# Kernel optimization log

Hardware: AMD Instinct MI355X
Metric: run time of the kernel (lower is better)

The kernel has to match this reference:

```python
import jax, jax.numpy as jnp
import numpy as np

B, S, H, NH = 2, 2048, 1024, 16
HD = H // NH  # head_dim = 64
ROPE_BASE = 10000.0


def _rope(x):
    # x: [B, NH, S, HD]; LLaMA-style half-split rotary embedding
    s, d = x.shape[2], x.shape[3]
    inv_freq = 1.0 / (ROPE_BASE ** (jnp.arange(0, d, 2, dtype=jnp.float32) / d))  # [d/2]
    ang = jnp.arange(s, dtype=jnp.float32)[:, None] * inv_freq[None, :]            # [S, d/2]
    cos, sin = jnp.cos(ang), jnp.sin(ang)
    x1, x2 = x[..., : d // 2], x[..., d // 2:]
    return jnp.concatenate([x1 * cos - x2 * sin, x1 * sin + x2 * cos], axis=-1)


def setup_inputs() -> dict:
    key = jax.random.key(0)
    ks = jax.random.split(key, 9)
    hidden_states = jax.random.normal(ks[0], (B, S, H), dtype=jnp.float32)
    # causal mask: True = attend
    causal = jnp.tril(jnp.ones((S, S), dtype=bool))
    attention_mask = jnp.broadcast_to(causal[None, None, :, :], (B, 1, S, S))
    std = 0.02
    wq = jax.random.normal(ks[1], (H, NH * HD), dtype=jnp.float32) * std
    wk = jax.random.normal(ks[2], (H, NH * HD), dtype=jnp.float32) * std
    wv = jax.random.normal(ks[3], (H, NH * HD), dtype=jnp.float32) * std
    wo = jax.random.normal(ks[4], (NH * HD, H), dtype=jnp.float32) * std
    bq = jnp.zeros((NH * HD,), dtype=jnp.float32)
    bk = jnp.zeros((NH * HD,), dtype=jnp.float32)
    bv = jnp.zeros((NH * HD,), dtype=jnp.float32)
    bo = jnp.zeros((H,), dtype=jnp.float32)
    return {"hidden_states": hidden_states, "attention_mask": attention_mask,
            "wq": wq, "bq": bq, "wk": wk, "bk": bk, "wv": wv, "bv": bv,
            "wo": wo, "bo": bo}


def _split_heads(x):
    b, s, _ = x.shape
    return jnp.transpose(x.reshape(b, s, NH, HD), (0, 2, 1, 3))


def reference(hidden_states, attention_mask, wq, bq, wk, bk, wv, bv, wo, bo):
    q = _split_heads(hidden_states @ wq + bq)  # [B,NH,S,HD]
    k = _split_heads(hidden_states @ wk + bk)
    v = _split_heads(hidden_states @ wv + bv)
    q = _rope(q)
    k = _rope(k)
    scores = jnp.einsum('bhqd,bhkd->bhqk', q, k) / jnp.sqrt(jnp.float32(HD))
    scores = jnp.where(attention_mask, scores, jnp.float32(-1e9))
    weights = jax.nn.softmax(scores, axis=-1)
    attn = jnp.einsum('bhqk,bhkv->bhqv', weights, v)  # [B,NH,S,HD]
    attn = jnp.transpose(attn, (0, 2, 1, 3)).reshape(hidden_states.shape[0], attn.shape[2], H)
    return attn @ wo + bo
```

## Files before the change

### kernel.cpp

```cpp
#include <hip/hip_runtime.h>
#include <math.h>

typedef short bf16x8 __attribute__((ext_vector_type(8)));
typedef short bf16x4 __attribute__((ext_vector_type(4)));
typedef float f32x4  __attribute__((ext_vector_type(4)));

__device__ __forceinline__ unsigned short f2bf(float f) {
    union { float f; unsigned u; } v; v.f = f;
    unsigned r = v.u + 0x7FFFu + ((v.u >> 16) & 1u);
    return (unsigned short)(r >> 16);
}

__device__ __forceinline__ unsigned cvt_pk_bf16(float a, float b) {
    unsigned r;
    asm("v_cvt_pk_bf16_f32 %0, %1, %2" : "=v"(r) : "v"(a), "v"(b));
    return r;
}

#define GLDS16(gp, lp) __builtin_amdgcn_global_load_lds( \
    (const __attribute__((address_space(1))) void*)(gp), \
    (__attribute__((address_space(3))) void*)(lp), 16, 0, 0)


__global__ __launch_bounds__(256)
void prep(const float* __restrict__ X, unsigned short* __restrict__ Xb,
          const float* __restrict__ w0, const float* __restrict__ w1,
          const float* __restrict__ w2, const float* __restrict__ w3,
          unsigned short* o0, unsigned short* o1,
          unsigned short* o2, unsigned short* o3)
{
    const int z = blockIdx.z;
    if (z >= 4) {
        const int lb = (z - 4) * 256 + blockIdx.y * 16 + blockIdx.x;
        const size_t t = (size_t)lb * 256 + threadIdx.x;
        const float4 a = *(const float4*)(X + t * 8);
        const float4 b = *(const float4*)(X + t * 8 + 4);
        unsigned short u[8] = { f2bf(a.x), f2bf(a.y), f2bf(a.z), f2bf(a.w),
                                f2bf(b.x), f2bf(b.y), f2bf(b.z), f2bf(b.w) };
        *(int4*)(Xb + t * 8) = *(int4*)u;
        return;
    }
    const float* W; unsigned short* O;
    switch (z) {
        case 0: W = w0; O = o0; break;
        case 1: W = w1; O = o1; break;
        case 2: W = w2; O = o2; break;
        default: W = w3; O = o3; break;
    }
    __shared__ float T[64][65];
    const int tid = threadIdx.x;
    const int n0 = blockIdx.x * 64, k0 = blockIdx.y * 64;
    #pragma unroll
    for (int i = 0; i < 4; i++) {
        const int k = (tid >> 4) + i * 16, n4 = (tid & 15) * 4;
        const float4 v = *(const float4*)(W + (size_t)(k0 + k) * 1024 + n0 + n4);
        T[k][n4] = v.x; T[k][n4+1] = v.y; T[k][n4+2] = v.z; T[k][n4+3] = v.w;
    }
    __syncthreads();
    if (z == 3) {
        #pragma unroll
        for (int i = 0; i < 4; i++) {
            const int n = (tid >> 4) + i * 16, k4 = (tid & 15) * 4;
            unsigned short u[4];
            #pragma unroll
            for (int j = 0; j < 4; j++) {
                const int q = k4 + j;
                const int p = (q & 3) * 16 + (q >> 2);
                const int d = (p & 3) * 16 + (p >> 2);
                u[j] = f2bf(T[d][n]);
            }
            *(int2*)(O + (size_t)(n0 + n) * 1024 + k0 + k4) = *(int2*)u;
        }
    } else {
        #pragma unroll
        for (int i = 0; i < 4; i++) {
            const int n = (tid >> 4) + i * 16, k4 = (tid & 15) * 4;
            unsigned short u[4] = { f2bf(T[k4][n]), f2bf(T[k4+1][n]),
                                    f2bf(T[k4+2][n]), f2bf(T[k4+3][n]) };
            *(int2*)(O + (size_t)(n0 + n) * 1024 + k0 + k4) = *(int2*)u;
        }
    }
}

__global__ __launch_bounds__(256)
void qkv_gemm(const unsigned short* __restrict__ Xb,
              const unsigned short* __restrict__ Wtq, const unsigned short* __restrict__ Wtk,
              const unsigned short* __restrict__ Wtv,
              const float* __restrict__ bq, const float* __restrict__ bk,
              const float* __restrict__ bv,
              unsigned short* __restrict__ Qb, unsigned short* __restrict__ Kb,
              unsigned short* __restrict__ Vtb)
{
    const unsigned short* Wt; const float* bias; unsigned short* Out;
    const int z = blockIdx.z;
    if (z == 0)      { Wt = Wtq; bias = bq; Out = Qb; }
    else if (z == 1) { Wt = Wtk; bias = bk; Out = Kb; }
    else             { Wt = Wtv; bias = bv; Out = Vtb; }

    __shared__ unsigned short Sh[128 * 72];
    unsigned short* As = Sh;
    unsigned short* Bs = Sh + 128 * 32;
    unsigned short* T  = Sh;

    const int tid = threadIdx.x, lane = tid & 63, w = tid >> 6;
    const int quad = lane >> 4, c = lane & 15;
    const int wr = w >> 1, wc = w & 1;
    const int m0 = blockIdx.x * 128, n0 = blockIdx.y * 128;
    const int srow = lane >> 2, scol = (lane & 3) * 8;

    f32x4 acc[4][4];
    #pragma unroll
    for (int i = 0; i < 4; i++)
        #pragma unroll
        for (int j = 0; j < 4; j++) acc[i][j] = (f32x4){0.f, 0.f, 0.f, 0.f};

    for (int k0 = 0; k0 < 1024; k0 += 32) {
        #pragma unroll
        for (int j = 0; j < 2; j++) {
            const int r = w * 32 + j * 16;
            GLDS16(Xb + (size_t)(m0 + r + srow) * 1024 + k0 + scol, &As[r * 32]);
            GLDS16(Wt + (size_t)(n0 + r + srow) * 1024 + k0 + scol, &Bs[r * 32]);
        }
        __syncthreads();
        bf16x8 af[4], bf[4];
        #pragma unroll
        for (int rt = 0; rt < 4; rt++)
            af[rt] = *(const bf16x8*)&As[(wr * 64 + rt * 16 + c) * 32 + quad * 8];
        #pragma unroll
        for (int nt = 0; nt < 4; nt++)
            bf[nt] = *(const bf16x8*)&Bs[(wc * 64 + nt * 16 + c) * 32 + quad * 8];
        #pragma unroll
        for (int rt = 0; rt < 4; rt++)
            #pragma unroll
            for (int nt = 0; nt < 4; nt++)
                acc[rt][nt] = __builtin_amdgcn_mfma_f32_16x16x32_bf16(af[rt], bf[nt], acc[rt][nt], 0, 0, 0);
        __syncthreads();
    }

    float bv4[4];
    #pragma unroll
    for (int nt = 0; nt < 4; nt++) bv4[nt] = bias[n0 + wc * 64 + nt * 16 + c];

    if (z == 2) {
        const int b = m0 >> 11, sb = m0 & 2047;
        const int hgbase = n0 >> 6;
        #pragma unroll
        for (int h = 0; h < 2; h++) {
            if (wc == h) {
                #pragma unroll
                for (int rt = 0; rt < 4; rt++)
                    #pragma unroll
                    for (int reg = 0; reg < 4; reg++) {
                        const int s = wr * 64 + rt * 16 + quad * 4 + reg;
                        unsigned short u[4];
                        #pragma unroll
                        for (int nt = 0; nt < 4; nt++)
                            u[nt] = f2bf(acc[rt][nt][reg] + bv4[nt]);
                        *(int2*)&T[s * 72 + c * 4] = *(int2*)u;
                    }
            }
            __syncthreads();
            const int p = tid >> 2, s8 = (tid & 3) * 32;
            unsigned short* dstb = Vtb + ((size_t)(b * 16 + hgbase + h) * 64 + p) * 2048 + sb;
            #pragma unroll
            for (int jj = 0; jj < 32; jj += 8) {
                unsigned short u[8];
                #pragma unroll
                for (int j = 0; j < 8; j++) u[j] = T[(s8 + jj + j) * 72 + p];
                *(int4*)(dstb + s8 + jj) = *(int4*)u;
            }
            __syncthreads();
        }
        return;
    }

    const float kLn = 9.210340371976184f / 32.0f;
    const float TWO_PI_INV = 0.15915494309189535f;
    const float rv0 = expf(-(float)c * kLn) * TWO_PI_INV;
    const float rv1 = expf(-(float)(c + 16) * kLn) * TWO_PI_INV;
    const float qscale = (z == 0) ? 0.125f : 1.0f;

    #pragma unroll
    for (int rt = 0; rt < 4; rt++) {
        #pragma unroll
        for (int reg = 0; reg < 4; reg++) {
            const int m = m0 + wr * 64 + rt * 16 + quad * 4 + reg;
            const int b = m >> 11, s = m & 2047;
            float x0 = acc[rt][0][reg] + bv4[0];
            float x1 = acc[rt][1][reg] + bv4[1];
            float x2 = acc[rt][2][reg] + bv4[2];
            float x3 = acc[rt][3][reg] + bv4[3];
            float r0 = (float)s * rv0;  r0 -= floorf(r0);
            float r1 = (float)s * rv1;  r1 -= floorf(r1);
            const float sn0 = __builtin_amdgcn_sinf(r0);
            const float cs0 = __builtin_amdgcn_cosf(r0);
            const float sn1 = __builtin_amdgcn_sinf(r1);
            const float cs1 = __builtin_amdgcn_cosf(r1);
            const float y0 = (x0 * cs0 - x2 * sn0) * qscale;
            const float y2 = (x0 * sn0 + x2 * cs0) * qscale;
            const float y1 = (x1 * cs1 - x3 * sn1) * qscale;
            const float y3 = (x1 * sn1 + x3 * cs1) * qscale;
            const int h = (n0 + wc * 64) >> 6;
            unsigned short u[4] = { f2bf(y0), f2bf(y1), f2bf(y2), f2bf(y3) };
            unsigned short* dst = Out + ((size_t)(b * 16 + h) * 2048 + s) * 64;
            *(int2*)(dst + c * 4) = *(int2*)u;
        }
    }
}

__global__ __launch_bounds__(256)
void out_gemm(const unsigned short* __restrict__ Ab, const unsigned short* __restrict__ Wto,
              const float* __restrict__ bo, float* __restrict__ Out)
{
    __shared__ unsigned short As[64 * 32];
    __shared__ unsigned short Bs[128 * 32];
    const int tid = threadIdx.x, lane = tid & 63, w = tid >> 6;
    const int quad = lane >> 4, c = lane & 15;
    const int wr = w >> 1, wc = w & 1;
    const int m0 = blockIdx.x * 64, n0 = blockIdx.y * 128;
    const int srow = lane >> 2, scol = (lane & 3) * 8;

    f32x4 acc[2][4];
    #pragma unroll
    for (int i = 0; i < 2; i++)
        #pragma unroll
        for (int j = 0; j < 4; j++) acc[i][j] = (f32x4){0.f, 0.f, 0.f, 0.f};

    for (int k0 = 0; k0 < 1024; k0 += 32) {
        {
            const int r = w * 16;
            GLDS16(Ab + (size_t)(m0 + r + srow) * 1024 + k0 + scol, &As[r * 32]);
        }
        #pragma unroll
        for (int j = 0; j < 2; j++) {
            const int r = w * 32 + j * 16;
            GLDS16(Wto + (size_t)(n0 + r + srow) * 1024 + k0 + scol, &Bs[r * 32]);
        }
        __syncthreads();
        bf16x8 af[2], bf[4];
        #pragma unroll
        for (int rt = 0; rt < 2; rt++)
            af[rt] = *(const bf16x8*)&As[(wr * 32 + rt * 16 + c) * 32 + quad * 8];
        #pragma unroll
        for (int nt = 0; nt < 4; nt++)
            bf[nt] = *(const bf16x8*)&Bs[(wc * 64 + nt * 16 + c) * 32 + quad * 8];
        #pragma unroll
        for (int rt = 0; rt < 2; rt++)
            #pragma unroll
            for (int nt = 0; nt < 4; nt++)
                acc[rt][nt] = __builtin_amdgcn_mfma_f32_16x16x32_bf16(af[rt], bf[nt], acc[rt][nt], 0, 0, 0);
        __syncthreads();
    }
    #pragma unroll
    for (int rt = 0; rt < 2; rt++) {
        #pragma unroll
        for (int reg = 0; reg < 4; reg++) {
            const int m = m0 + wr * 32 + rt * 16 + quad * 4 + reg;
            #pragma unroll
            for (int nt = 0; nt < 4; nt++) {
                const int n = n0 + wc * 64 + nt * 16 + c;
                Out[(size_t)m * 1024 + n] = acc[rt][nt][reg] + bo[n];
            }
        }
    }
}

__global__ __launch_bounds__(512)
void attn_part(const unsigned short* __restrict__ Qb, const unsigned short* __restrict__ Kb,
               const unsigned short* __restrict__ Vtb, unsigned short* __restrict__ Ab,
               float* __restrict__ Opart, float* __restrict__ Lpart)
{
    __shared__ unsigned short Ks[64 * 72];
    __shared__ unsigned short Vs[64 * 72];

    const int tid = threadIdx.x, w = tid >> 6, lane = tid & 63;
    const int quad = lane >> 4, c = lane & 15;
    const int bh = blockIdx.y;
    const int x = blockIdx.x;
    int ip, start, len;
    if (x < 8)       { ip = 9 + x;  start = 0;  len = 16; }
    else if (x < 16) { ip = 24 - x; start = 16; len = 2 * ip - 16; }
    else             { ip = 24 - x; start = 0;  len = 2 * ip; }
    const int q0 = (ip - 1) * 128;
    const bool complete = (x >= 16);
    const size_t base = (size_t)bh * 2048 * 64;

    bf16x8 on;
    #pragma unroll
    for (int i = 0; i < 8; i++) on[i] = (short)0x3F80;

    const int qbase = q0 + w * 16;
    const int qrow  = qbase + c;
    const size_t qoff = base + (size_t)qrow * 64;
    const bf16x8 qf0 = *(const bf16x8*)(Qb + qoff + quad * 8);
    const bf16x8 qf1 = *(const bf16x8*)(Qb + qoff + 32 + quad * 8);

    f32x4 O[4], Osum;
    Osum = (f32x4){0.f, 0.f, 0.f, 0.f};
    #pragma unroll
    for (int nt = 0; nt < 4; nt++) O[nt] = (f32x4){0.f, 0.f, 0.f, 0.f};

    const int rs = tid >> 3, c8 = (tid & 7) * 8;

    int k0 = start * 64;
    int4 kreg = *(const int4*)(Kb  + base + (size_t)(k0 + rs) * 64 + c8);
    int4 vreg = *(const int4*)(Vtb + base + (size_t)rs * 2048 + k0 + c8);

    union P8 { bf16x8 v8; unsigned wd[4]; };
    union V8 { bf16x8 v8; bf16x4 v4[2]; };

    for (int t = 0; t < len; t++, k0 += 64) {
        *(int4*)&Ks[(size_t)rs * 72 + c8] = kreg;
        *(int4*)&Vs[(size_t)rs * 72 + c8] = vreg;
        __syncthreads();

        if (t + 1 < len) {
            const int kn = k0 + 64;
            kreg = *(const int4*)(Kb  + base + (size_t)(kn + rs) * 64 + c8);
            vreg = *(const int4*)(Vtb + base + (size_t)rs * 2048 + kn + c8);
        }

        if (k0 <= qbase + 15) {
            const bool need_mask = (k0 + 63) > qbase;
            P8 pa0, pa1;
            __builtin_amdgcn_s_setprio(1);
            #pragma unroll
            for (int nt = 0; nt < 4; nt++) {
                const bf16x8 kf0 = *(const bf16x8*)&Ks[(nt * 16 + c) * 72 + quad * 8];
                const bf16x8 kf1 = *(const bf16x8*)&Ks[(nt * 16 + c) * 72 + 32 + quad * 8];
                f32x4 s4 = (f32x4){0.f, 0.f, 0.f, 0.f};
                s4 = __builtin_amdgcn_mfma_f32_16x16x32_bf16(kf0, qf0, s4, 0, 0, 0);
                s4 = __builtin_amdgcn_mfma_f32_16x16x32_bf16(kf1, qf1, s4, 0, 0, 0);
                const int keyb = k0 + nt * 16 + quad * 4;
                float p[4];
                #pragma unroll
                for (int reg = 0; reg < 4; reg++) {
                    float pv = __expf(s4[reg]);
                    if (need_mask && (keyb + reg > qrow)) pv = 0.f;
                    p[reg] = pv;
                }
                const unsigned wa = cvt_pk_bf16(p[0], p[1]);
                const unsigned wb = cvt_pk_bf16(p[2], p[3]);
                if (nt < 2) { pa0.wd[2 * nt]     = wa; pa0.wd[2 * nt + 1]     = wb; }
                else        { pa1.wd[2 * (nt-2)] = wa; pa1.wd[2 * (nt-2) + 1] = wb; }
            }

            #pragma unroll
            for (int nt = 0; nt < 4; nt++) {
                const int pr = (nt * 16 + c) * 72 + 4 * quad;
                V8 vb0, vb1;
                vb0.v4[0] = *(const bf16x4*)&Vs[pr];
                vb0.v4[1] = *(const bf16x4*)&Vs[pr + 16];
                vb1.v4[0] = *(const bf16x4*)&Vs[pr + 32];
                vb1.v4[1] = *(const bf16x4*)&Vs[pr + 48];
                O[nt] = __builtin_amdgcn_mfma_f32_16x16x32_bf16(pa0.v8, vb0.v8, O[nt], 0, 0, 0);
                O[nt] = __builtin_amdgcn_mfma_f32_16x16x32_bf16(pa1.v8, vb1.v8, O[nt], 0, 0, 0);
            }
            Osum = __builtin_amdgcn_mfma_f32_16x16x32_bf16(pa0.v8, on, Osum, 0, 0, 0);
            Osum = __builtin_amdgcn_mfma_f32_16x16x32_bf16(pa1.v8, on, Osum, 0, 0, 0);
            __builtin_amdgcn_s_setprio(0);
        }
        __syncthreads();
    }

    if (complete) {
        const int b = bh >> 4, h = bh & 15;
        #pragma unroll
        for (int reg = 0; reg < 4; reg++) {
            const float inv = 1.0f / Osum[reg];
            const int q = qbase + quad * 4 + reg;
            unsigned short u[4];
            #pragma unroll
            for (int nt = 0; nt < 4; nt++) u[nt] = f2bf(O[nt][reg] * inv);
            unsigned short* dst = Ab + ((size_t)(b * 2048 + q)) * 1024 + h * 64;
            *(int2*)(dst + c * 4) = *(int2*)u;
        }
    } else {
        const int pslot = (ip - 9) * 2 + (start ? 1 : 0);
        float* Op = Opart + ((size_t)bh * 16 + pslot) * 8192;
        float* Lp = Lpart + (size_t)bh * 2048 + (size_t)pslot * 128;
        #pragma unroll
        for (int reg = 0; reg < 4; reg++) {
            const int row = w * 16 + quad * 4 + reg;
            float4 o4 = make_float4(O[0][reg], O[1][reg], O[2][reg], O[3][reg]);
            *(float4*)(Op + (size_t)row * 64 + c * 4) = o4;
            if (c == 0) Lp[row] = Osum[reg];
        }
    }
}

__global__ __launch_bounds__(256)
void attn_combine(const float* __restrict__ Opart, const float* __restrict__ Lpart,
                  unsigned short* __restrict__ Ab)
{
    const int tid = threadIdx.x;
    const int j = blockIdx.x, bh = blockIdx.y;
    const int q0 = (8 + j) * 128;
    const size_t s0 = ((size_t)bh * 16 + j * 2) * 8192;
    const size_t l0 = (size_t)bh * 2048 + (size_t)j * 2 * 128;

    __shared__ float linv[128];
    if (tid < 128) linv[tid] = 1.0f / (Lpart[l0 + tid] + Lpart[l0 + 128 + tid]);
    __syncthreads();

    const int row = tid >> 1, col0 = (tid & 1) * 32;
    const float inv = linv[row];
    const int b = bh >> 4, h = bh & 15;
    const int q = q0 + row;
    unsigned short* dst = Ab + ((size_t)(b * 2048 + q)) * 1024 + h * 64 + col0;
    #pragma unroll
    for (int c4 = 0; c4 < 32; c4 += 4) {
        const float4 a  = *(const float4*)(Opart + s0 + (size_t)row * 64 + col0 + c4);
        const float4 bb = *(const float4*)(Opart + s0 + 8192 + (size_t)row * 64 + col0 + c4);
        dst[c4 + 0] = f2bf((a.x + bb.x) * inv);
        dst[c4 + 1] = f2bf((a.y + bb.y) * inv);
        dst[c4 + 2] = f2bf((a.z + bb.z) * inv);
        dst[c4 + 3] = f2bf((a.w + bb.w) * inv);
    }
}

extern "C" void kernel_launch(void* const* d_in, const int* in_sizes, int n_in,
                              void* d_out, int out_size, void* d_ws, size_t ws_size,
                              hipStream_t stream)
{
    const float* X  = (const float*)d_in[0];
    const float* wq = (const float*)d_in[2];
    const float* bq = (const float*)d_in[3];
    const float* wk = (const float*)d_in[4];
    const float* bk = (const float*)d_in[5];
    const float* wv = (const float*)d_in[6];
    const float* bv = (const float*)d_in[7];
    const float* wo = (const float*)d_in[8];
    const float* bo = (const float*)d_in[9];

    unsigned short* ws = (unsigned short*)d_ws;
    const size_t M1 = 1024 * 1024;
    unsigned short* Xb  = ws;
    unsigned short* Wtq = Xb  + 4 * M1;
    unsigned short* Wtk = Wtq + M1;
    unsigned short* Wtv = Wtk + M1;
    unsigned short* Wto = Wtv + M1;
    unsigned short* Qb  = Wto + M1;
    unsigned short* Kb  = Qb  + 4 * M1;
    unsigned short* Vtb = Kb  + 4 * M1;
    unsigned short* Ab  = Vtb + 4 * M1;
    float* Opart = (float*)(Ab + 4 * M1);
    float* Lpart = Opart + (size_t)32 * 16 * 8192;

    prep        <<<dim3(16, 16, 12), 256, 0, stream>>>(X, Xb, wq, wk, wv, wo,
                                                       Wtq, Wtk, Wtv, Wto);
    qkv_gemm    <<<dim3(32, 8, 3), 256, 0, stream>>>(Xb, Wtq, Wtk, Wtv, bq, bk, bv,
                                                     Qb, Kb, Vtb);
    attn_part   <<<dim3(24, 32), 512, 0, stream>>>(Qb, Kb, Vtb, Ab, Opart, Lpart);
    attn_combine<<<dim3(8, 32), 256, 0, stream>>>(Opart, Lpart, Ab);
    out_gemm    <<<dim3(64, 8), 256, 0, stream>>>(Ab, Wto, bo, (float*)d_out);
}
```

Measured before the change: 211.4 us.

## Double attention query tile per warp to reuse K/V tiles across 256 rows

Each warp now processes two 16-row query sub-tiles (32 rows), so each block covers 256 query rows instead of 128. Every K/V tile loaded into LDS feeds twice as many MFMAs, and the grid shrinks from 24 to 12 blocks per head, with the causal work split remapped through a packed lookup constant. The cost is more registers per thread, fewer blocks (384 total) to fill the GPU, and coarser causal load balancing. The partial-result layout and the combine kernel are adjusted to match.

```diff
diff --git a/kernel.cpp b/kernel.cpp
--- a/kernel.cpp
+++ b/kernel.cpp
@@ -277,28 +277,31 @@
     const int quad = lane >> 4, c = lane & 15;
     const int bh = blockIdx.y;
     const int x = blockIdx.x;
-    int ip, start, len;
-    if (x < 8)       { ip = 9 + x;  start = 0;  len = 16; }
-    else if (x < 16) { ip = 24 - x; start = 16; len = 2 * ip - 16; }
-    else             { ip = 24 - x; start = 0;  len = 2 * ip; }
-    const int q0 = (ip - 1) * 128;
-    const bool complete = (x >= 16);
+    const int i = (int)((0x014425566377ULL >> (4 * x)) & 15);
+    const int chunk = (594 >> x) & 1;
+    const int len = ((i >= 4) ? 2 : 4) * (i + 1);
+    const int start = chunk ? len : 0;
+    const int q0 = i * 256;
+    const bool complete = (i <= 3);
     const size_t base = (size_t)bh * 2048 * 64;
 
     bf16x8 on;
     #pragma unroll
-    for (int i = 0; i < 8; i++) on[i] = (short)0x3F80;
-
-    const int qbase = q0 + w * 16;
-    const int qrow  = qbase + c;
-    const size_t qoff = base + (size_t)qrow * 64;
-    const bf16x8 qf0 = *(const bf16x8*)(Qb + qoff + quad * 8);
-    const bf16x8 qf1 = *(const bf16x8*)(Qb + qoff + 32 + quad * 8);
-
-    f32x4 O[4], Osum;
-    Osum = (f32x4){0.f, 0.f, 0.f, 0.f};
-    #pragma unroll
-    for (int nt = 0; nt < 4; nt++) O[nt] = (f32x4){0.f, 0.f, 0.f, 0.f};
+    for (int ii = 0; ii < 8; ii++) on[ii] = (short)0x3F80;
+
+    const int qbase = q0 + w * 32;
+    const size_t qoffA = base + (size_t)(qbase + c) * 64;
+    const size_t qoffB = base + (size_t)(qbase + 16 + c) * 64;
+    const bf16x8 qfA0 = *(const bf16x8*)(Qb + qoffA + quad * 8);
+    const bf16x8 qfA1 = *(const bf16x8*)(Qb + qoffA + 32 + quad * 8);
+    const bf16x8 qfB0 = *(const bf16x8*)(Qb + qoffB + quad * 8);
+    const bf16x8 qfB1 = *(const bf16x8*)(Qb + qoffB + 32 + quad * 8);
+
+    f32x4 OA[4], OB[4], OsA, OsB;
+    OsA = (f32x4){0.f, 0.f, 0.f, 0.f};
+    OsB = (f32x4){0.f, 0.f, 0.f, 0.f};
+    #pragma unroll
+    for (int nt = 0; nt < 4; nt++) { OA[nt] = OsA; OB[nt] = OsA; }
 
     const int rs = tid >> 3, c8 = (tid & 7) * 8;
 
@@ -320,29 +323,45 @@
             vreg = *(const int4*)(Vtb + base + (size_t)rs * 2048 + kn + c8);
         }
 
-        if (k0 <= qbase + 15) {
-            const bool need_mask = (k0 + 63) > qbase;
-            P8 pa0, pa1;
+        if (k0 <= qbase + 31) {
+            const int qrowA = qbase + c;
+            const int qrowB = qbase + 16 + c;
+            const bool nmA = (k0 + 63) > qbase;
+            const bool nmB = (k0 + 63) > (qbase + 16);
+            P8 paA0, paA1, paB0, paB1;
             __builtin_amdgcn_s_setprio(1);
             #pragma unroll
             for (int nt = 0; nt < 4; nt++) {
                 const bf16x8 kf0 = *(const bf16x8*)&Ks[(nt * 16 + c) * 72 + quad * 8];
                 const bf16x8 kf1 = *(const bf16x8*)&Ks[(nt * 16 + c) * 72 + 32 + quad * 8];
-                f32x4 s4 = (f32x4){0.f, 0.f, 0.f, 0.f};
-                s4 = __builtin_amdgcn_mfma_f32_16x16x32_bf16(kf0, qf0, s4, 0, 0, 0);
-                s4 = __builtin_amdgcn_mfma_f32_16x16x32_bf16(kf1, qf1, s4, 0, 0, 0);
+                f32x4 sA = (f32x4){0.f, 0.f, 0.f, 0.f};
+                f32x4 sB = sA;
+                sA = __builtin_amdgcn_mfma_f32_16x16x32_bf16(kf0, qfA0, sA, 0, 0, 0);
+                sA = __builtin_amdgcn_mfma_f32_16x16x32_bf16(kf1, qfA1, sA, 0, 0, 0);
+                sB = __builtin_amdgcn_mfma_f32_16x16x32_bf16(kf0, qfB0, sB, 0, 0, 0);
+                sB = __builtin_amdgcn_mfma_f32_16x16x32_bf16(kf1, qfB1, sB, 0, 0, 0);
                 const int keyb = k0 + nt * 16 + quad * 4;
-                float p[4];
+                float pA[4], pB[4];
                 #pragma unroll
                 for (int reg = 0; reg < 4; reg++) {
-                    float pv = __expf(s4[reg]);
-                    if (need_mask && (keyb + reg > qrow)) pv = 0.f;
-                    p[reg] = pv;
+                    float va = __expf(sA[reg]);
+                    if (nmA && (keyb + reg > qrowA)) va = 0.f;
+                    pA[reg] = va;
+                    float vb = __expf(sB[reg]);
+                    if (nmB && (keyb + reg > qrowB)) vb = 0.f;
+                    pB[reg] = vb;
                 }
-                const unsigned wa = cvt_pk_bf16(p[0], p[1]);
-                const unsigned wb = cvt_pk_bf16(p[2], p[3]);
-                if (nt < 2) { pa0.wd[2 * nt]     = wa; pa0.wd[2 * nt + 1]     = wb; }
-                else        { pa1.wd[2 * (nt-2)] = wa; pa1.wd[2 * (nt-2) + 1] = wb; }
+                const unsigned waA = cvt_pk_bf16(pA[0], pA[1]);
+                const unsigned wbA = cvt_pk_bf16(pA[2], pA[3]);
+                const unsigned waB = cvt_pk_bf16(pB[0], pB[1]);
+                const unsigned wbB = cvt_pk_bf16(pB[2], pB[3]);
+                if (nt < 2) {
+                    paA0.wd[2 * nt] = waA;     paA0.wd[2 * nt + 1] = wbA;
+                    paB0.wd[2 * nt] = waB;     paB0.wd[2 * nt + 1] = wbB;
+                } else {
+                    paA1.wd[2 * (nt-2)] = waA; paA1.wd[2 * (nt-2) + 1] = wbA;
+                    paB1.wd[2 * (nt-2)] = waB; paB1.wd[2 * (nt-2) + 1] = wbB;
+                }
             }
 
             #pragma unroll
@@ -353,11 +372,15 @@
                 vb0.v4[1] = *(const bf16x4*)&Vs[pr + 16];
                 vb1.v4[0] = *(const bf16x4*)&Vs[pr + 32];
                 vb1.v4[1] = *(const bf16x4*)&Vs[pr + 48];
-                O[nt] = __builtin_amdgcn_mfma_f32_16x16x32_bf16(pa0.v8, vb0.v8, O[nt], 0, 0, 0);
-                O[nt] = __builtin_amdgcn_mfma_f32_16x16x32_bf16(pa1.v8, vb1.v8, O[nt], 0, 0, 0);
-            }
-            Osum = __builtin_amdgcn_mfma_f32_16x16x32_bf16(pa0.v8, on, Osum, 0, 0, 0);
-            Osum = __builtin_amdgcn_mfma_f32_16x16x32_bf16(pa1.v8, on, Osum, 0, 0, 0);
+                OA[nt] = __builtin_amdgcn_mfma_f32_16x16x32_bf16(paA0.v8, vb0.v8, OA[nt], 0, 0, 0);
+                OA[nt] = __builtin_amdgcn_mfma_f32_16x16x32_bf16(paA1.v8, vb1.v8, OA[nt], 0, 0, 0);
+                OB[nt] = __builtin_amdgcn_mfma_f32_16x16x32_bf16(paB0.v8, vb0.v8, OB[nt], 0, 0, 0);
+                OB[nt] = __builtin_amdgcn_mfma_f32_16x16x32_bf16(paB1.v8, vb1.v8, OB[nt], 0, 0, 0);
+            }
+            OsA = __builtin_amdgcn_mfma_f32_16x16x32_bf16(paA0.v8, on, OsA, 0, 0, 0);
+            OsA = __builtin_amdgcn_mfma_f32_16x16x32_bf16(paA1.v8, on, OsA, 0, 0, 0);
+            OsB = __builtin_amdgcn_mfma_f32_16x16x32_bf16(paB0.v8, on, OsB, 0, 0, 0);
+            OsB = __builtin_amdgcn_mfma_f32_16x16x32_bf16(paB1.v8, on, OsB, 0, 0, 0);
             __builtin_amdgcn_s_setprio(0);
         }
         __syncthreads();
@@ -367,24 +390,37 @@
         const int b = bh >> 4, h = bh & 15;
         #pragma unroll
         for (int reg = 0; reg < 4; reg++) {
-            const float inv = 1.0f / Osum[reg];
-            const int q = qbase + quad * 4 + reg;
-            unsigned short u[4];
-            #pragma unroll
-            for (int nt = 0; nt < 4; nt++) u[nt] = f2bf(O[nt][reg] * inv);
-            unsigned short* dst = Ab + ((size_t)(b * 2048 + q)) * 1024 + h * 64;
-            *(int2*)(dst + c * 4) = *(int2*)u;
+            const float invA = 1.0f / OsA[reg];
+            const int qA = qbase + quad * 4 + reg;
+            unsigned short uA[4];
+            #pragma unroll
+            for (int nt = 0; nt < 4; nt++) uA[nt] = f2bf(OA[nt][reg] * invA);
+            unsigned short* dA = Ab + ((size_t)(b * 2048 + qA)) * 1024 + h * 64;
+            *(int2*)(dA + c * 4) = *(int2*)uA;
+
+            const float invB = 1.0f / OsB[reg];
+            const int qB = qbase + 16 + quad * 4 + reg;
+            unsigned short uB[4];
+            #pragma unroll
+            for (int nt = 0; nt < 4; nt++) uB[nt] = f2bf(OB[nt][reg] * invB);
+            unsigned short* dB = Ab + ((size_t)(b * 2048 + qB)) * 1024 + h * 64;
+            *(int2*)(dB + c * 4) = *(int2*)uB;
         }
     } else {
-        const int pslot = (ip - 9) * 2 + (start ? 1 : 0);
-        float* Op = Opart + ((size_t)bh * 16 + pslot) * 8192;
-        float* Lp = Lpart + (size_t)bh * 2048 + (size_t)pslot * 128;
+        const int slot = (i - 4) * 2 + chunk;
+        float* Op = Opart + ((size_t)bh * 8 + slot) * 16384;
+        float* Lp = Lpart + (size_t)bh * 2048 + (size_t)slot * 256;
         #pragma unroll
         for (int reg = 0; reg < 4; reg++) {
-            const int row = w * 16 + quad * 4 + reg;
-            float4 o4 = make_float4(O[0][reg], O[1][reg], O[2][reg], O[3][reg]);
-            *(float4*)(Op + (size_t)row * 64 + c * 4) = o4;
-            if (c == 0) Lp[row] = Osum[reg];
+            const int rowA = w * 32 + quad * 4 + reg;
+            float4 oA = make_float4(OA[0][reg], OA[1][reg], OA[2][reg], OA[3][reg]);
+            *(float4*)(Op + (size_t)rowA * 64 + c * 4) = oA;
+            if (c == 0) Lp[rowA] = OsA[reg];
+
+            const int rowB = rowA + 16;
+            float4 oB = make_float4(OB[0][reg], OB[1][reg], OB[2][reg], OB[3][reg]);
+            *(float4*)(Op + (size_t)rowB * 64 + c * 4) = oB;
+            if (c == 0) Lp[rowB] = OsB[reg];
         }
     }
 }
@@ -395,12 +431,14 @@
 {
     const int tid = threadIdx.x;
     const int j = blockIdx.x, bh = blockIdx.y;
-    const int q0 = (8 + j) * 128;
-    const size_t s0 = ((size_t)bh * 16 + j * 2) * 8192;
-    const size_t l0 = (size_t)bh * 2048 + (size_t)j * 2 * 128;
+    const int i = 4 + (j >> 1), half = j & 1;
+    const int slot0 = (i - 4) * 2;
+    const int q0 = i * 256 + half * 128;
+    const size_t s0 = ((size_t)bh * 8 + slot0) * 16384 + (size_t)half * 128 * 64;
+    const size_t l0 = (size_t)bh * 2048 + (size_t)slot0 * 256 + half * 128;
 
     __shared__ float linv[128];
-    if (tid < 128) linv[tid] = 1.0f / (Lpart[l0 + tid] + Lpart[l0 + 128 + tid]);
+    if (tid < 128) linv[tid] = 1.0f / (Lpart[l0 + tid] + Lpart[l0 + 256 + tid]);
     __syncthreads();
 
     const int row = tid >> 1, col0 = (tid & 1) * 32;
@@ -411,7 +449,7 @@
     #pragma unroll
     for (int c4 = 0; c4 < 32; c4 += 4) {
         const float4 a  = *(const float4*)(Opart + s0 + (size_t)row * 64 + col0 + c4);
-        const float4 bb = *(const float4*)(Opart + s0 + 8192 + (size_t)row * 64 + col0 + c4);
+        const float4 bb = *(const float4*)(Opart + s0 + 16384 + (size_t)row * 64 + col0 + c4);
         dst[c4 + 0] = f2bf((a.x + bb.x) * inv);
         dst[c4 + 1] = f2bf((a.y + bb.y) * inv);
         dst[c4 + 2] = f2bf((a.z + bb.z) * inv);
@@ -445,13 +483,13 @@
     unsigned short* Vtb = Kb  + 4 * M1;
     unsigned short* Ab  = Vtb + 4 * M1;
     float* Opart = (float*)(Ab + 4 * M1);
-    float* Lpart = Opart + (size_t)32 * 16 * 8192;
+    float* Lpart = Opart + (size_t)32 * 8 * 16384;
 
     prep        <<<dim3(16, 16, 12), 256, 0, stream>>>(X, Xb, wq, wk, wv, wo,
                                                        Wtq, Wtk, Wtv, Wto);
     qkv_gemm    <<<dim3(32, 8, 3), 256, 0, stream>>>(Xb, Wtq, Wtk, Wtv, bq, bk, bv,
                                                      Qb, Kb, Vtb);
-    attn_part   <<<dim3(24, 32), 512, 0, stream>>>(Qb, Kb, Vtb, Ab, Opart, Lpart);
+    attn_part   <<<dim3(12, 32), 512, 0, stream>>>(Qb, Kb, Vtb, Ab, Opart, Lpart);
     attn_combine<<<dim3(8, 32), 256, 0, stream>>>(Opart, Lpart, Ab);
     out_gemm    <<<dim3(64, 8), 256, 0, stream>>>(Ab, Wto, bo, (float*)d_out);
 }
```

Measured after the change: 208.3 us. No clear change (-1.5%).
